# Optimization experiments

Hardware: AMD Instinct MI355X
Metric: run time of the kernel (lower is better)

The kernel has to match this reference:

```python
import jax, jax.numpy as jnp
import numpy as np

B, N, D, H, O, A, L = 128, 100, 2048, 1024, 1600, 400, 2048


def _mlp(x, w1, b1, w2, b2, w3, b3):
    h = jax.nn.relu(x @ w1 + b1)
    h = jax.nn.relu(h @ w2 + b2)
    return jax.nn.softmax(h @ w3 + b3, axis=2)  # softmax over class dim (dim=2)


def setup_inputs() -> dict:
    key = jax.random.key(0)
    ks = jax.random.split(key, 18)

    def lin(kw, fan_in, fan_out):
        s = 1.0 / np.sqrt(fan_in)
        return jax.random.normal(kw, (fan_in, fan_out), jnp.float32) * s

    x = jax.random.normal(ks[0], (B, N, D), jnp.float32)
    num_descs = jax.random.randint(ks[1], (B,), 0, N, jnp.int32)
    label_img = jnp.sort(jax.random.randint(ks[2], (L,), 0, B, jnp.int32))
    obj_labels = jax.random.randint(ks[3], (L,), 0, O)
    att_labels = jax.random.randint(ks[4], (L,), 0, A)

    inp = dict(x=x, num_descs=num_descs, label_img=label_img,
               obj_labels=obj_labels, att_labels=att_labels,
               w1o=lin(ks[5], D, H), b1o=jnp.zeros((H,), jnp.float32),
               w2o=lin(ks[6], H, H), b2o=jnp.zeros((H,), jnp.float32),
               w3o=lin(ks[7], H, O), b3o=jnp.zeros((O,), jnp.float32),
               w1a=lin(ks[8], D, H), b1a=jnp.zeros((H,), jnp.float32),
               w2a=lin(ks[9], H, H), b2a=jnp.zeros((H,), jnp.float32),
               w3a=lin(ks[10], H, A), b3a=jnp.zeros((A,), jnp.float32))
    return inp


def reference(x, num_descs, label_img, obj_labels, att_labels,
              w1o, b1o, w2o, b2o, w3o, b3o,
              w1a, b1a, w2a, b2a, w3a, b3a):
    po = _mlp(x, w1o, b1o, w2o, b2o, w3o, b3o)  # [B, N, O]
    pa = _mlp(x, w1a, b1a, w2a, b2a, w3a, b3a)  # [B, N, A]

    rows = jnp.arange(po.shape[1])  # [N]
    # per-label gather of the prob column for its object/attribute class -> [L, N]
    p_obj = po[label_img[:, None], rows[None, :], obj_labels[:, None]]
    p_att = pa[label_img[:, None], rows[None, :], att_labels[:, None]]
    # ragged unpad (descs beyond num_descs[img] excluded from argmax)
    valid = rows[None, :] < num_descs[label_img][:, None]
    score = jnp.where(valid, p_obj * p_att, -jnp.inf)
    desc = jnp.argmax(score, axis=1)  # [L]

    obj_dists = po[label_img, desc, :]  # [L, O]
    att_dists = pa[label_img, desc, :]  # [L, A]
    return (obj_dists, att_dists)
```

## Files before the change

kernel.cpp:

```cpp
#include <hip/hip_runtime.h>
#include <hip/hip_bf16.h>
#include <math.h>

#define Bq 128
#define Nq 100
#define Dq 2048
#define Hq 1024
#define Oq 1600
#define Aq 400
#define Lq 2048
#define Mq (Bq * Nq)
#define OqP 1664
#define AqP 512

typedef __attribute__((ext_vector_type(8))) short bf16x8;
typedef __attribute__((ext_vector_type(16))) float f32x16;
typedef unsigned short ushort;


__device__ __forceinline__ void split1(float v, ushort& h, ushort& l) {
    __hip_bfloat16 bh = __float2bfloat16(v);
    float fh = __bfloat162float(bh);
    __hip_bfloat16 bl = __float2bfloat16(v - fh);
    h = __builtin_bit_cast(ushort, bh);
    l = __builtin_bit_cast(ushort, bl);
}

__device__ __forceinline__ void gl_lds16(const ushort* g, ushort* lds) {
    __builtin_amdgcn_global_load_lds(
        (const __attribute__((address_space(1))) unsigned int*)g,
        (__attribute__((address_space(3))) unsigned int*)lds,
        16, 0, 0);
}

__global__ void build_offsets(const int* __restrict__ num_descs,
                              int* __restrict__ off, int* __restrict__ mc,
                              int* __restrict__ rowmap)
{
    __shared__ int cnt[Bq];
    __shared__ int offs[Bq + 1];
    const int t = threadIdx.x;
    int nd = num_descs[t];
    nd = nd < 0 ? 0 : (nd > Nq ? Nq : nd);
    const int c = nd < 1 ? 1 : nd;
    cnt[t] = c;
    __syncthreads();
    if (t == 0) {
        int s = 0;
        for (int i = 0; i < Bq; i++) { offs[i] = s; s += cnt[i]; }
        offs[Bq] = s;
        mc[0] = s;
        mc[1] = (s + 127) & ~127;
    }
    __syncthreads();
    off[t] = offs[t];
    for (int i = t; i < Mq; i += Bq) rowmap[i] = -1;
    __syncthreads();
    const int o = offs[t];
    for (int n = 0; n < c; n++) rowmap[o + n] = t * Nq + n;
}

__global__ void split_compact(const float* __restrict__ x,
                              const int* __restrict__ rowmap,
                              const int* __restrict__ mc,
                              ushort* __restrict__ hi, ushort* __restrict__ lo)
{
    const int KB = Dq / 16;
    const int wid = (blockIdx.x * blockDim.x + threadIdx.x) >> 6;
    const int lane = threadIdx.x & 63;
    const int rt = wid / KB;
    const int kb = wid - rt * KB;
    if (rt * 32 >= mc[1]) return;
    const int crow = rt * 32 + (lane & 31);
    const int k = kb * 16 + (lane >> 5) * 8;
    const int orig = (crow < mc[0]) ? rowmap[crow] : -1;
    ushort h[8], l[8];
    if (orig < 0) {
#pragma unroll
        for (int j = 0; j < 8; j++) { h[j] = 0; l[j] = 0; }
    } else {
        const float* src = x + (size_t)orig * Dq + k;
        float4 v0 = *(const float4*)(src);
        float4 v1 = *(const float4*)(src + 4);
        float v[8] = {v0.x, v0.y, v0.z, v0.w, v1.x, v1.y, v1.z, v1.w};
#pragma unroll
        for (int j = 0; j < 8; j++) split1(v[j], h[j], l[j]);
    }
    const size_t a = (size_t)wid * 512 + (size_t)lane * 8;
    *(bf16x8*)(hi + a) = *(bf16x8*)h;
    *(bf16x8*)(lo + a) = *(bf16x8*)l;
}

struct TSeg { const float* W; ushort* Th; ushort* Tl; int K; int N; int gx; int base; };
struct TSegs { TSeg s[6]; };

__global__ void tsplit_all(TSegs a)
{
    const int id = blockIdx.x;
    TSeg sg = a.s[5];
#pragma unroll
    for (int i = 4; i >= 0; i--) if (id < a.s[i + 1].base) sg = a.s[i];
    const int local = id - sg.base;
    const int bn = (local % sg.gx) * 32;
    const int bk = (local / sg.gx) * 32;
    const int KB = sg.K >> 4;

    __shared__ float t[32][33];
    const int tx = threadIdx.x & 31, ty = threadIdx.x >> 5;
#pragma unroll
    for (int i = 0; i < 4; i++) {
        const int k = bk + ty + i * 8, n = bn + tx;
        t[ty + i * 8][tx] = (n < sg.N) ? sg.W[(size_t)k * sg.N + n] : 0.f;
    }
    __syncthreads();

    const int wave = threadIdx.x >> 6;
    const int lane = threadIdx.x & 63;
    const int kc = wave & 1;
    const int hl = wave >> 1;
    const int nloc = lane & 31;
    const int kloc = kc * 16 + (lane >> 5) * 8;
    ushort v8[8];
#pragma unroll
    for (int e = 0; e < 8; e++) {
        ushort h, l;
        split1(t[kloc + e][nloc], h, l);
        v8[e] = hl ? l : h;
    }
    const size_t chunk = (size_t)((bn >> 5)) * KB + (bk >> 4) + kc;
    ushort* dst = (hl ? sg.Tl : sg.Th) + chunk * 512 + (size_t)lane * 8;
    *(bf16x8*)dst = *(bf16x8*)v8;
}

struct GArgs {
    const ushort* Ah; const ushort* Al;
    const ushort* Bh; const ushort* Bl;
    const float* bias;
    float* Cf; ushort* Ch; ushort* Cl;
    int K, Npad, Nreal, ldc, mode;
};

__global__ __launch_bounds__(256, 2) void gemm_split(GArgs g0, GArgs g1,
                                                     const int* __restrict__ mcp,
                                                     int nct0, int nct)
{
    const int ny = mcp[1] >> 7;
    const int nact = nct * ny;
    const int hw = blockIdx.x;
    if (hw >= nact) return;
    const int q = nact >> 3, r = nact & 7, xcd = hw & 7, pos = hw >> 3;
    const int L = (xcd < r ? xcd * (q + 1) : r * (q + 1) + (xcd - r) * q) + pos;
    const int by = L / nct;
    const int ct = L - by * nct;

    const GArgs g = (ct < nct0) ? g0 : g1;
    const int bm = by * 128;
    const int bn = (ct < nct0 ? ct : ct - nct0) * 128;

    const int KB = g.K >> 4;

    __shared__ __align__(16) ushort sAh[8192];
    __shared__ __align__(16) ushort sAl[8192];
    __shared__ __align__(16) ushort sBh[8192];
    __shared__ __align__(16) ushort sBl[8192];

    const int tid  = threadIdx.x;
    const int wave = tid >> 6;
    const int lane = tid & 63;
    const int wmi = (wave >> 1) * 2;
    const int wni = (wave & 1) * 2;
    const int l31  = lane & 31;
    const int half = lane >> 5;

    const ushort* gAh = g.Ah + ((size_t)(bm / 32 + wave) * KB) * 512 + lane * 8;
    const ushort* gAl = g.Al + ((size_t)(bm / 32 + wave) * KB) * 512 + lane * 8;
    const ushort* gBh = g.Bh + ((size_t)(bn / 32 + wave) * KB) * 512 + lane * 8;
    const ushort* gBl = g.Bl + ((size_t)(bn / 32 + wave) * KB) * 512 + lane * 8;

    f32x16 acc[2][2] = {};

    auto STAGE = [&](int c) {
        const size_t go = (size_t)c * 512;
        const int ls = ((c & 3) << 11) + (wave << 9);
        gl_lds16(gAh + go, &sAh[ls]);
        gl_lds16(gAl + go, &sAl[ls]);
        gl_lds16(gBh + go, &sBh[ls]);
        gl_lds16(gBl + go, &sBl[ls]);
    };

    auto PHASE = [&](int c, int stage_c, int drain) {
        const int slot = (c & 3) << 11;
        bf16x8 ah[2], al[2], bh[2], bl[2];
#pragma unroll
        for (int i = 0; i < 2; i++) {
            const int sa = slot + (wmi + i) * 512 + lane * 8;
            const int sb = slot + (wni + i) * 512 + lane * 8;
            ah[i] = *(const bf16x8*)&sAh[sa];
            al[i] = *(const bf16x8*)&sAl[sa];
            bh[i] = *(const bf16x8*)&sBh[sb];
            bl[i] = *(const bf16x8*)&sBl[sb];
        }
        if (stage_c >= 0) STAGE(stage_c);
        __builtin_amdgcn_s_setprio(1);
#pragma unroll
        for (int i = 0; i < 2; i++)
#pragma unroll
            for (int j = 0; j < 2; j++) {
                acc[i][j] = __builtin_amdgcn_mfma_f32_32x32x16_bf16(ah[i], bh[j], acc[i][j], 0, 0, 0);
                acc[i][j] = __builtin_amdgcn_mfma_f32_32x32x16_bf16(ah[i], bl[j], acc[i][j], 0, 0, 0);
                acc[i][j] = __builtin_amdgcn_mfma_f32_32x32x16_bf16(al[i], bh[j], acc[i][j], 0, 0, 0);
            }
        __builtin_amdgcn_s_setprio(0);
        if (drain == 8)      asm volatile("s_waitcnt vmcnt(8)" ::: "memory");
        else if (drain == 4) asm volatile("s_waitcnt vmcnt(4)" ::: "memory");
        else if (drain == 0) asm volatile("s_waitcnt vmcnt(0)" ::: "memory");
        if (drain >= 0) {
            asm volatile("s_waitcnt lgkmcnt(0)" ::: "memory");
            asm volatile("s_barrier" ::: "memory");
        }
    };

    STAGE(0); STAGE(1); STAGE(2);
    asm volatile("s_waitcnt vmcnt(8)" ::: "memory");
    asm volatile("s_barrier" ::: "memory");

    for (int c = 0; c < KB - 3; ++c) PHASE(c, c + 3, 8);
    PHASE(KB - 3, -1, 4);
    PHASE(KB - 2, -1, 0);
    PHASE(KB - 1, -1, -1);

    const int KC = g.ldc >> 4;
#pragma unroll
    for (int j = 0; j < 2; j++) {
        const int col = bn + (wni + j) * 32 + l31;
        if (col < g.Nreal) {
            const float bv = g.bias[col];
#pragma unroll
            for (int i = 0; i < 2; i++) {
#pragma unroll
                for (int r = 0; r < 16; r++) {
                    const int row = bm + (wmi + i) * 32 + (r & 3) + 8 * (r >> 2) + 4 * half;
                    float v = acc[i][j][r] + bv;
                    if (g.mode == 1) {
                        v = fmaxf(v, 0.f);
                        ushort h, l;
                        split1(v, h, l);
                        const size_t chunk = (size_t)(row >> 5) * KC + (col >> 4);
                        const size_t adr = chunk * 512
                            + (size_t)((row & 31) + 32 * ((col >> 3) & 1)) * 8 + (col & 7);
                        g.Ch[adr] = h;
                        g.Cl[adr] = l;
                    } else {
                        g.Cf[(size_t)row * g.ldc + col] = v;
                    }
                }
            }
        }
    }
}

__global__ void softmax_stats2(const float* __restrict__ Zo, const float* __restrict__ Za,
                               const int* __restrict__ mc,
                               float* __restrict__ mxo, float* __restrict__ smo,
                               float* __restrict__ mxa, float* __restrict__ sma)
{
    const int r = blockIdx.x;
    if (r >= mc[0]) return;
    const float* Z; int ncols; float* mx; float* sm;
    if (blockIdx.y == 0) { Z = Zo; ncols = Oq; mx = mxo; sm = smo; }
    else                 { Z = Za; ncols = Aq; mx = mxa; sm = sma; }
    const float* row = Z + (size_t)r * ncols;
    __shared__ float red[256];
    float m = -INFINITY;
    for (int c = threadIdx.x; c < ncols; c += 256) m = fmaxf(m, row[c]);
    red[threadIdx.x] = m;
    __syncthreads();
    for (int s = 128; s > 0; s >>= 1) {
        if (threadIdx.x < s) red[threadIdx.x] = fmaxf(red[threadIdx.x], red[threadIdx.x + s]);
        __syncthreads();
    }
    m = red[0];
    __syncthreads();
    float su = 0.f;
    for (int c = threadIdx.x; c < ncols; c += 256) su += expf(row[c] - m);
    red[threadIdx.x] = su;
    __syncthreads();
    for (int s = 128; s > 0; s >>= 1) {
        if (threadIdx.x < s) red[threadIdx.x] += red[threadIdx.x + s];
        __syncthreads();
    }
    if (threadIdx.x == 0) { mx[r] = m; sm[r] = red[0]; }
}

__global__ void argmax_gather(
    const float* __restrict__ Zo, const float* __restrict__ Za,
    const float* __restrict__ mxo, const float* __restrict__ smo,
    const float* __restrict__ mxa, const float* __restrict__ sma,
    const int* __restrict__ label_img, const int* __restrict__ num_descs,
    const int* __restrict__ obj_labels, const int* __restrict__ att_labels,
    const int* __restrict__ off, float* __restrict__ out)
{
    const int l = blockIdx.x;
    const int b = label_img[l];
    const int nd = num_descs[b];
    const int r0 = off[b];
    const int t = threadIdx.x;

    __shared__ float ss[128];
    __shared__ int   si[128];
    if (t < 128) {
        float score = -INFINITY;
        if (t < Nq && t < nd) {
            const int r = r0 + t;
            const float po = expf(Zo[(size_t)r * Oq + obj_labels[l]] - mxo[r]) / smo[r];
            const float pa = expf(Za[(size_t)r * Aq + att_labels[l]] - mxa[r]) / sma[r];
            score = po * pa;
        }
        ss[t] = score;
        si[t] = t;
    }
    __syncthreads();
    for (int s = 64; s > 0; s >>= 1) {
        if (t < s) {
            const float s2 = ss[t + s];
            const int   i2 = si[t + s];
            if (s2 > ss[t] || (s2 == ss[t] && i2 < si[t])) { ss[t] = s2; si[t] = i2; }
        }
        __syncthreads();
    }
    const int r = r0 + si[0];

    const float mo = mxo[r], so = smo[r];
    const float* zo = Zo + (size_t)r * Oq;
    float* oo = out + (size_t)l * Oq;
    for (int c = t; c < Oq; c += 256)
        oo[c] = expf(zo[c] - mo) / so;

    const float ma = mxa[r], sa = sma[r];
    const float* za = Za + (size_t)r * Aq;
    float* oa = out + (size_t)Lq * Oq + (size_t)l * Aq;
    for (int c = t; c < Aq; c += 256)
        oa[c] = expf(za[c] - ma) / sa;
}

extern "C" void kernel_launch(void* const* d_in, const int* in_sizes, int n_in,
                              void* d_out, int out_size, void* d_ws, size_t ws_size,
                              hipStream_t stream)
{
    const float* x          = (const float*)d_in[0];
    const int*   num_descs  = (const int*)d_in[1];
    const int*   label_img  = (const int*)d_in[2];
    const int*   obj_labels = (const int*)d_in[3];
    const int*   att_labels = (const int*)d_in[4];
    const float* w1o = (const float*)d_in[5];  const float* b1o = (const float*)d_in[6];
    const float* w2o = (const float*)d_in[7];  const float* b2o = (const float*)d_in[8];
    const float* w3o = (const float*)d_in[9];  const float* b3o = (const float*)d_in[10];
    const float* w1a = (const float*)d_in[11]; const float* b1a = (const float*)d_in[12];
    const float* w2a = (const float*)d_in[13]; const float* b2a = (const float*)d_in[14];
    const float* w3a = (const float*)d_in[15]; const float* b3a = (const float*)d_in[16];
    float* out = (float*)d_out;

    char* p = (char*)d_ws;
    auto carve = [&](size_t bytes) { char* q = p; p += (bytes + 255) & ~(size_t)255; return q; };

    char* bufA = carve((size_t)Mq * Dq * 2 * 2);
    char* bufB = carve((size_t)Mq * Hq * 2 * 2 * 2);
    ushort* w1oth = (ushort*)carve((size_t)Hq * Dq * 2);  ushort* w1otl = (ushort*)carve((size_t)Hq * Dq * 2);
    ushort* w1ath = (ushort*)carve((size_t)Hq * Dq * 2);  ushort* w1atl = (ushort*)carve((size_t)Hq * Dq * 2);
    ushort* w2oth = (ushort*)carve((size_t)Hq * Hq * 2);  ushort* w2otl = (ushort*)carve((size_t)Hq * Hq * 2);
    ushort* w2ath = (ushort*)carve((size_t)Hq * Hq * 2);  ushort* w2atl = (ushort*)carve((size_t)Hq * Hq * 2);
    ushort* w3oth = (ushort*)carve((size_t)OqP * Hq * 2); ushort* w3otl = (ushort*)carve((size_t)OqP * Hq * 2);
    ushort* w3ath = (ushort*)carve((size_t)AqP * Hq * 2); ushort* w3atl = (ushort*)carve((size_t)AqP * Hq * 2);
    float* mxo = (float*)carve(Mq * 4); float* smo = (float*)carve(Mq * 4);
    float* mxa = (float*)carve(Mq * 4); float* sma = (float*)carve(Mq * 4);
    int* off    = (int*)carve(Bq * 4);
    int* mc     = (int*)carve(4 * 4);
    int* rowmap = (int*)carve(Mq * 4);

    ushort* xh = (ushort*)bufA;
    ushort* xl = xh + (size_t)Mq * Dq;
    ushort* h2oh = (ushort*)bufA;
    ushort* h2ol = h2oh + (size_t)Mq * Hq;
    ushort* h2ah = h2ol + (size_t)Mq * Hq;
    ushort* h2al = h2ah + (size_t)Mq * Hq;
    ushort* h1oh = (ushort*)bufB;
    ushort* h1ol = h1oh + (size_t)Mq * Hq;
    ushort* h1ah = h1ol + (size_t)Mq * Hq;
    ushort* h1al = h1ah + (size_t)Mq * Hq;
    float* z3o = (float*)bufB;
    float* z3a = z3o + (size_t)Mq * Oq;

    build_offsets<<<1, 128, 0, stream>>>(num_descs, off, mc, rowmap);
    split_compact<<<(Mq / 32) * (Dq / 16) / 4, 256, 0, stream>>>(x, rowmap, mc, xh, xl);

    {
        TSegs ts;
        int base = 0;
        auto seg = [&](const float* W, ushort* Th, ushort* Tl, int K, int N, int Npad) {
            TSeg s; s.W = W; s.Th = Th; s.Tl = Tl; s.K = K; s.N = N;
            s.gx = Npad / 32; s.base = base; base += (Npad / 32) * (K / 32); return s;
        };
        ts.s[0] = seg(w1o, w1oth, w1otl, Dq, Hq, Hq);
        ts.s[1] = seg(w1a, w1ath, w1atl, Dq, Hq, Hq);
        ts.s[2] = seg(w2o, w2oth, w2otl, Hq, Hq, Hq);
        ts.s[3] = seg(w2a, w2ath, w2atl, Hq, Hq, Hq);
        ts.s[4] = seg(w3o, w3oth, w3otl, Hq, Oq, OqP);
        ts.s[5] = seg(w3a, w3ath, w3atl, Hq, Aq, AqP);
        tsplit_all<<<base, 256, 0, stream>>>(ts);
    }

    {
        GArgs go = { xh, xl, w1oth, w1otl, b1o, nullptr, h1oh, h1ol, Dq, Hq, Hq, Hq, 1 };
        GArgs ga = { xh, xl, w1ath, w1atl, b1a, nullptr, h1ah, h1al, Dq, Hq, Hq, Hq, 1 };
        gemm_split<<<16 * (Mq / 128), 256, 0, stream>>>(go, ga, mc, 8, 16);
    }
    {
        GArgs go = { h1oh, h1ol, w2oth, w2otl, b2o, nullptr, h2oh, h2ol, Hq, Hq, Hq, Hq, 1 };
        GArgs ga = { h1ah, h1al, w2ath, w2atl, b2a, nullptr, h2ah, h2al, Hq, Hq, Hq, Hq, 1 };
        gemm_split<<<16 * (Mq / 128), 256, 0, stream>>>(go, ga, mc, 8, 16);
    }
    {
        GArgs go = { h2oh, h2ol, w3oth, w3otl, b3o, z3o, nullptr, nullptr, Hq, OqP, Oq, Oq, 0 };
        GArgs ga = { h2ah, h2al, w3ath, w3atl, b3a, z3a, nullptr, nullptr, Hq, AqP, Aq, Aq, 0 };
        gemm_split<<<(OqP / 128 + AqP / 128) * (Mq / 128), 256, 0, stream>>>(go, ga, mc,
                                                                            OqP / 128,
                                                                            OqP / 128 + AqP / 128);
    }

    softmax_stats2<<<dim3(Mq, 2), 256, 0, stream>>>(z3o, z3a, mc, mxo, smo, mxa, sma);
    argmax_gather<<<Lq, 256, 0, stream>>>(z3o, z3a, mxo, smo, mxa, sma,
                                          label_img, num_descs, obj_labels, att_labels, off, out);
}
```

Baseline: 578.0 us.

## Cut GEMM LDS pipeline to three stages for higher occupancy; coalesce x split

The split-bf16 GEMM now uses a 3-slot instead of 4-slot LDS ring, which shrinks shared memory per block from 64KB to 48KB, and launch bounds are raised to 3 blocks per CU. Prefetch depth drops from 3 chunks ahead to 2, with matching waitcnt changes. The x split/compaction kernel now stages a 32x64 tile through shared memory so that each row is read contiguously before it is split and written in fragment layout. This trades latency hiding for occupancy, and the higher block count per CU may also force register spills.

```diff
diff --git a/kernel.cpp b/kernel.cpp
--- a/kernel.cpp
+++ b/kernel.cpp
@@ -60,33 +60,49 @@
     for (int n = 0; n < c; n++) rowmap[o + n] = t * Nq + n;
 }
 
-__global__ void split_compact(const float* __restrict__ x,
+__global__ __launch_bounds__(256) void split_compact(const float* __restrict__ x,
                               const int* __restrict__ rowmap,
                               const int* __restrict__ mc,
                               ushort* __restrict__ hi, ushort* __restrict__ lo)
 {
     const int KB = Dq / 16;
-    const int wid = (blockIdx.x * blockDim.x + threadIdx.x) >> 6;
-    const int lane = threadIdx.x & 63;
-    const int rt = wid / KB;
-    const int kb = wid - rt * KB;
+    const int nbc = Dq / 64;
+    const int rt = blockIdx.x / nbc;
+    const int bc = (blockIdx.x - rt * nbc) * 64;
     if (rt * 32 >= mc[1]) return;
-    const int crow = rt * 32 + (lane & 31);
-    const int k = kb * 16 + (lane >> 5) * 8;
-    const int orig = (crow < mc[0]) ? rowmap[crow] : -1;
+
+    __shared__ float t[32][66];
+    const int tid = threadIdx.x;
+    {
+        const int row = tid >> 3;
+        const int coff = (tid & 7) * 8;
+        const int crow = rt * 32 + row;
+        const int orig = (crow < mc[0]) ? rowmap[crow] : -1;
+        float v[8];
+        if (orig < 0) {
+#pragma unroll
+            for (int e = 0; e < 8; e++) v[e] = 0.f;
+        } else {
+            const float* src = x + (size_t)orig * Dq + bc + coff;
+            float4 v0 = *(const float4*)(src);
+            float4 v1 = *(const float4*)(src + 4);
+            v[0] = v0.x; v[1] = v0.y; v[2] = v0.z; v[3] = v0.w;
+            v[4] = v1.x; v[5] = v1.y; v[6] = v1.z; v[7] = v1.w;
+        }
+#pragma unroll
+        for (int e = 0; e < 8; e++) t[row][coff + e] = v[e];
+    }
+    __syncthreads();
+
+    const int wave = tid >> 6;
+    const int lane = tid & 63;
+    const int r32 = lane & 31;
+    const int cl = wave * 16 + (lane >> 5) * 8;
     ushort h[8], l[8];
-    if (orig < 0) {
-#pragma unroll
-        for (int j = 0; j < 8; j++) { h[j] = 0; l[j] = 0; }
-    } else {
-        const float* src = x + (size_t)orig * Dq + k;
-        float4 v0 = *(const float4*)(src);
-        float4 v1 = *(const float4*)(src + 4);
-        float v[8] = {v0.x, v0.y, v0.z, v0.w, v1.x, v1.y, v1.z, v1.w};
-#pragma unroll
-        for (int j = 0; j < 8; j++) split1(v[j], h[j], l[j]);
-    }
-    const size_t a = (size_t)wid * 512 + (size_t)lane * 8;
+#pragma unroll
+    for (int e = 0; e < 8; e++) split1(t[r32][cl + e], h[e], l[e]);
+    const size_t wid = (size_t)rt * KB + (bc >> 4) + wave;
+    const size_t a = wid * 512 + (size_t)lane * 8;
     *(bf16x8*)(hi + a) = *(bf16x8*)h;
     *(bf16x8*)(lo + a) = *(bf16x8*)l;
 }
@@ -140,7 +156,7 @@
     int K, Npad, Nreal, ldc, mode;
 };
 
-__global__ __launch_bounds__(256, 2) void gemm_split(GArgs g0, GArgs g1,
+__global__ __launch_bounds__(256, 3) void gemm_split(GArgs g0, GArgs g1,
                                                      const int* __restrict__ mcp,
                                                      int nct0, int nct)
 {
@@ -159,10 +175,10 @@
 
     const int KB = g.K >> 4;
 
-    __shared__ __align__(16) ushort sAh[8192];
-    __shared__ __align__(16) ushort sAl[8192];
-    __shared__ __align__(16) ushort sBh[8192];
-    __shared__ __align__(16) ushort sBl[8192];
+    __shared__ __align__(16) ushort sAh[6144];
+    __shared__ __align__(16) ushort sAl[6144];
+    __shared__ __align__(16) ushort sBh[6144];
+    __shared__ __align__(16) ushort sBl[6144];
 
     const int tid  = threadIdx.x;
     const int wave = tid >> 6;
@@ -181,7 +197,7 @@
 
     auto STAGE = [&](int c) {
         const size_t go = (size_t)c * 512;
-        const int ls = ((c & 3) << 11) + (wave << 9);
+        const int ls = (c % 3) * 2048 + (wave << 9);
         gl_lds16(gAh + go, &sAh[ls]);
         gl_lds16(gAl + go, &sAl[ls]);
         gl_lds16(gBh + go, &sBh[ls]);
@@ -189,7 +205,7 @@
     };
 
     auto PHASE = [&](int c, int stage_c, int drain) {
-        const int slot = (c & 3) << 11;
+        const int slot = (c % 3) * 2048;
         bf16x8 ah[2], al[2], bh[2], bl[2];
 #pragma unroll
         for (int i = 0; i < 2; i++) {
@@ -211,8 +227,7 @@
                 acc[i][j] = __builtin_amdgcn_mfma_f32_32x32x16_bf16(al[i], bh[j], acc[i][j], 0, 0, 0);
             }
         __builtin_amdgcn_s_setprio(0);
-        if (drain == 8)      asm volatile("s_waitcnt vmcnt(8)" ::: "memory");
-        else if (drain == 4) asm volatile("s_waitcnt vmcnt(4)" ::: "memory");
+        if (drain == 4)      asm volatile("s_waitcnt vmcnt(4)" ::: "memory");
         else if (drain == 0) asm volatile("s_waitcnt vmcnt(0)" ::: "memory");
         if (drain >= 0) {
             asm volatile("s_waitcnt lgkmcnt(0)" ::: "memory");
@@ -220,12 +235,11 @@
         }
     };
 
-    STAGE(0); STAGE(1); STAGE(2);
-    asm volatile("s_waitcnt vmcnt(8)" ::: "memory");
+    STAGE(0); STAGE(1);
+    asm volatile("s_waitcnt vmcnt(4)" ::: "memory");
     asm volatile("s_barrier" ::: "memory");
 
-    for (int c = 0; c < KB - 3; ++c) PHASE(c, c + 3, 8);
-    PHASE(KB - 3, -1, 4);
+    for (int c = 0; c < KB - 2; ++c) PHASE(c, c + 2, 4);
     PHASE(KB - 2, -1, 0);
     PHASE(KB - 1, -1, -1);
 
@@ -391,7 +405,7 @@
     float* z3a = z3o + (size_t)Mq * Oq;
 
     build_offsets<<<1, 128, 0, stream>>>(num_descs, off, mc, rowmap);
-    split_compact<<<(Mq / 32) * (Dq / 16) / 4, 256, 0, stream>>>(x, rowmap, mc, xh, xl);
+    split_compact<<<(Mq / 32) * (Dq / 64), 256, 0, stream>>>(x, rowmap, mc, xh, xl);
 
     {
         TSegs ts;
```

Measured after the change: 638.2 us. +10.4%, slower.
